# Kernel tuning notes

Hardware: AMD Instinct MI355X
Metric: run time of the kernel (lower is better)

The kernel has to match this reference:

```python
import jax, jax.numpy as jnp
import numpy as np

D_MODEL = 1024
N_EXPERTS = 8
TOP_K = 2
BOTTLENECK = 64
B, S = 2, 4096
ADAPTER_SCALE = 0.5


def setup_inputs() -> dict:
    key = jax.random.key(0)
    ks = jax.random.split(key, 8)
    sd = 0.02
    x = jax.random.normal(ks[0], (B, S, D_MODEL), dtype=jnp.float32)
    w_gate = jax.random.normal(ks[1], (D_MODEL, N_EXPERTS), dtype=jnp.float32) * sd
    w_noise = jax.random.normal(ks[2], (D_MODEL, N_EXPERTS), dtype=jnp.float32) * sd
    Wd = jax.random.normal(ks[3], (N_EXPERTS, D_MODEL, BOTTLENECK), dtype=jnp.float32) * sd
    bd = jnp.zeros((N_EXPERTS, BOTTLENECK), dtype=jnp.float32)
    Wu = jax.random.normal(ks[4], (N_EXPERTS, BOTTLENECK, D_MODEL), dtype=jnp.float32) * sd
    bu = jnp.zeros((N_EXPERTS, D_MODEL), dtype=jnp.float32)
    return {"x": x, "w_gate": w_gate, "w_noise": w_noise,
            "Wd": Wd, "bd": bd, "Wu": Wu, "bu": bu}


def _moe_forward(x, w_gate, w_noise, Wd, bd, Wu, bu):
    b, s, d = x.shape
    xf = x.reshape(-1, d)                      # [T, D] flattened tokens
    T = xf.shape[0]

    # --- noisy top-k gating (eval mode: no noise added, logits = clean) ---
    clean_logits = xf @ w_gate                 # [T, E]
    logits = clean_logits
    k1 = min(TOP_K + 1, N_EXPERTS)
    top_logits, top_idx = jax.lax.top_k(logits, k1)
    top_k_logits = top_logits[:, :TOP_K]       # [T, k]
    top_k_idx = top_idx[:, :TOP_K]             # [T, k]
    top_k_gates = jax.nn.softmax(top_k_logits, axis=-1)
    rows = jnp.arange(T)[:, None]
    gates = jnp.zeros((T, N_EXPERTS), dtype=top_k_gates.dtype)
    gates = gates.at[rows, top_k_idx].set(top_k_gates)  # sparse gate matrix [T, E]

    # --- experts (AdaptFormer adapters): dense compute, sparse combine ---
    # mathematically identical to SparseDispatcher dispatch/combine:
    # out[t] = sum_e gates[t,e] * expert_e(x[t])  (gates zero off top-k)
    h = jax.nn.relu(jnp.einsum('td,edb->teb', xf, Wd) + bd[None, :, :])  # [T,E,b]
    y = jnp.einsum('teb,ebd->ted', h, Wu) + bu[None, :, :]               # [T,E,D]
    y = ADAPTER_SCALE * y
    out = jnp.einsum('te,ted->td', gates, y)   # weighted combine (index_add equiv)
    return out.reshape(b, s, d)


def reference(x, w_gate, w_noise, Wd, bd, Wu, bu):
    return _moe_forward(x, w_gate, w_noise, Wd, bd, Wu, bu)
```

## Files before the change

kernel.cpp:

```cpp
#include <hip/hip_runtime.h>
#include <stdint.h>

#define T_TOK 8192
#define DM    1024
#define NE    8
#define BOT   64
#define HD    512
#define HD2   576
#define PW    8
#define NPREP (T_TOK / PW)

typedef __attribute__((ext_vector_type(8))) short bf16x8;
typedef __attribute__((ext_vector_type(4))) short bf16x4;
typedef __attribute__((ext_vector_type(4))) float f32x4;

__device__ __forceinline__ ushort f2bf(float f) {
  union { float f; uint32_t u; } v; v.f = f;
  uint32_t r = (v.u + 0x7fffu + ((v.u >> 16) & 1u)) >> 16;
  return (ushort)r;
}

__global__ __launch_bounds__(256, 2)
void prep_cvt_kernel(const float* __restrict__ x, const float* __restrict__ wg,
                     const float* __restrict__ Wd, const float* __restrict__ Wu,
                     const float* __restrict__ bu,
                     ushort* __restrict__ Xb, float* __restrict__ sg,
                     ushort* __restrict__ H2, ushort* __restrict__ WdT,
                     ushort* __restrict__ Wu2T) {
  __shared__ float part[4][PW][NE];
  __shared__ float sgl[PW][NE];
  __shared__ ushort tl[64][72];
  if (blockIdx.x < NPREP) {
    const int lane = threadIdx.x & 63;
    const int w    = threadIdx.x >> 6;
    const int t0   = blockIdx.x * PW;
    const int dd   = w * 256 + lane * 4;
    float4 wgr[4][2];
    #pragma unroll
    for (int j = 0; j < 4; ++j) {
      wgr[j][0] = *(const float4*)(wg + (size_t)(dd + j) * NE);
      wgr[j][1] = *(const float4*)(wg + (size_t)(dd + j) * NE + 4);
    }
    const int ebit = ((lane & 1) << 2) | (lane & 2) | ((lane >> 2) & 1);
    const float* xp = x + (size_t)t0 * DM + dd;
    float4 xv = *(const float4*)xp;
    #pragma unroll
    for (int tk = 0; tk < PW; ++tk) {
      float4 nxt = {};
      if (tk + 1 < PW) nxt = *(const float4*)(xp + (size_t)(tk + 1) * DM);
      bf16x4 xb;
      xb[0] = (short)f2bf(xv.x); xb[1] = (short)f2bf(xv.y);
      xb[2] = (short)f2bf(xv.z); xb[3] = (short)f2bf(xv.w);
      *(bf16x4*)(Xb + (size_t)(t0 + tk) * DM + dd) = xb;
      float a[NE] = {};
      const float* xs = (const float*)&xv;
      #pragma unroll
      for (int j = 0; j < 4; ++j) {
        const float xj = xs[j];
        const float* wr = (const float*)&wgr[j][0];
        #pragma unroll
        for (int e = 0; e < NE; ++e) a[e] += xj * wr[e];
      }
      float t0v[4];
      #pragma unroll
      for (int j = 0; j < 4; ++j) {
        float send = (lane & 1) ? a[j] : a[j + 4];
        float keep = (lane & 1) ? a[j + 4] : a[j];
        t0v[j] = keep + __shfl_xor(send, 1);
      }
      float t1v[2];
      #pragma unroll
      for (int j = 0; j < 2; ++j) {
        float send = (lane & 2) ? t0v[j] : t0v[j + 2];
        float keep = (lane & 2) ? t0v[j + 2] : t0v[j];
        t1v[j] = keep + __shfl_xor(send, 2);
      }
      {
        float send = (lane & 4) ? t1v[0] : t1v[1];
        float keep = (lane & 4) ? t1v[1] : t1v[0];
        float t2 = keep + __shfl_xor(send, 4);
        t2 += __shfl_xor(t2, 8);
        t2 += __shfl_xor(t2, 16);
        t2 += __shfl_xor(t2, 32);
        if (lane < NE) part[w][tk][ebit] = t2;
      }
      xv = nxt;
    }
    __syncthreads();
    const int tid = threadIdx.x;
    if (tid < PW) {
      float lg[NE];
      #pragma unroll
      for (int e = 0; e < NE; ++e)
        lg[e] = part[0][tid][e] + part[1][tid][e] + part[2][tid][e] + part[3][tid][e];
      int e0 = 0; float l0 = lg[0];
      #pragma unroll
      for (int e = 1; e < NE; ++e) if (lg[e] > l0) { l0 = lg[e]; e0 = e; }
      int e1 = -1; float l1 = -3.4e38f;
      #pragma unroll
      for (int e = 0; e < NE; ++e) if (e != e0 && lg[e] > l1) { l1 = lg[e]; e1 = e; }
      const float p1  = __expf(l1 - l0);
      const float inv = 1.f / (1.f + p1);
      const float g0 = 0.5f * inv, g1 = 0.5f * p1 * inv;
      float g[NE];
      #pragma unroll
      for (int e = 0; e < NE; ++e) g[e] = (e == e0) ? g0 : ((e == e1) ? g1 : 0.f);
      #pragma unroll
      for (int e = 0; e < NE; ++e) sgl[tid][e] = g[e];
      *(float4*)(sg + (size_t)(t0 + tid) * NE)     = *(float4*)&g[0];
      *(float4*)(sg + (size_t)(t0 + tid) * NE + 4) = *(float4*)&g[4];
    }
    __syncthreads();
    if (tid < PW * 8) {
      const int tk = tid >> 3, ch = tid & 7;
      bf16x8 v;
      #pragma unroll
      for (int k = 0; k < 8; ++k)
        v[k] = (ch == 0) ? (short)f2bf(sgl[tk][k]) : (short)0;
      *(bf16x8*)(H2 + (size_t)(t0 + tk) * HD2 + HD + ch * 8) = v;
    }
  } else {
    const int rr = threadIdx.x >> 2;
    const int cc = (threadIdx.x & 3) * 16;
    const int bx = blockIdx.x - NPREP;
    if (bx < 128) {
      const int e  = bx >> 4;
      const int d0 = (bx & 15) * 64;
      const float* src = Wd + ((size_t)e * DM + d0 + rr) * BOT + cc;
      #pragma unroll
      for (int i = 0; i < 4; ++i) {
        float4 v = *(const float4*)(src + i * 4);
        tl[rr][cc + i * 4 + 0] = f2bf(v.x);
        tl[rr][cc + i * 4 + 1] = f2bf(v.y);
        tl[rr][cc + i * 4 + 2] = f2bf(v.z);
        tl[rr][cc + i * 4 + 3] = f2bf(v.w);
      }
      __syncthreads();
      bf16x8 o0, o1;
      #pragma unroll
      for (int k = 0; k < 8; ++k) o0[k] = (short)tl[cc + k][rr];
      #pragma unroll
      for (int k = 0; k < 8; ++k) o1[k] = (short)tl[cc + 8 + k][rr];
      ushort* dst = WdT + ((size_t)e * BOT + rr) * DM + d0 + cc;
      *(bf16x8*)dst       = o0;
      *(bf16x8*)(dst + 8) = o1;
    } else {
      const int b2 = bx - 128;
      const int n0 = (b2 >> 4) * 64;
      const int d0 = (b2 & 15) * 64;
      const int n  = n0 + rr;
      #pragma unroll
      for (int i = 0; i < 4; ++i) {
        float4 v;
        if (n < HD)           v = *(const float4*)(Wu + (size_t)n * DM + d0 + cc + i * 4);
        else if (n < HD + NE) v = *(const float4*)(bu + (size_t)(n - HD) * DM + d0 + cc + i * 4);
        else { v.x = 0.f; v.y = 0.f; v.z = 0.f; v.w = 0.f; }
        tl[rr][cc + i * 4 + 0] = f2bf(v.x);
        tl[rr][cc + i * 4 + 1] = f2bf(v.y);
        tl[rr][cc + i * 4 + 2] = f2bf(v.z);
        tl[rr][cc + i * 4 + 3] = f2bf(v.w);
      }
      __syncthreads();
      bf16x8 o0, o1;
      #pragma unroll
      for (int k = 0; k < 8; ++k) o0[k] = (short)tl[cc + k][rr];
      #pragma unroll
      for (int k = 0; k < 8; ++k) o1[k] = (short)tl[cc + 8 + k][rr];
      ushort* dst = Wu2T + (size_t)(d0 + rr) * HD2 + n0 + cc;
      *(bf16x8*)dst       = o0;
      *(bf16x8*)(dst + 8) = o1;
    }
  }
}

template <int EPI, int NKT, int NBX>
__global__ __launch_bounds__(256)
void gemm_bt(const ushort* __restrict__ A, const ushort* __restrict__ B,
             const float* __restrict__ sg, const float* __restrict__ bd,
             ushort* __restrict__ Hout, float* __restrict__ Cout, int nwg) {
  constexpr int K = NKT * 64;
  __shared__ __attribute__((aligned(16))) ushort sA[3][128 * 64];
  __shared__ __attribute__((aligned(16))) ushort sB[3][64 * 64];
  const int lane = threadIdx.x & 63;
  const int w    = threadIdx.x >> 6;
  const int lb = (blockIdx.x % 8) * (nwg / 8) + blockIdx.x / 8;
  const int tile_m = (lb / NBX) * 128;
  const int tile_n = (lb % NBX) * 64;
  const int wm = (w >> 1) * 64;
  const int wn = (w & 1) * 32;
  const int sr = lane >> 3;
  const int sc = ((lane & 7) * 8) ^ (sr << 3);
  const int lr = lane & 15;
  const int kg = lane >> 4;
  const int swz = (lr & 7) << 3;
  f32x4 acc[4][2] = {};

#define STAGE(buf, kt) do {                                                       \
    const int k0_ = (kt) << 6;                                                    \
    _Pragma("unroll")                                                             \
    for (int c = 0; c < 4; ++c) {                                                 \
      const ushort* ga = A + (size_t)(tile_m + w * 32 + c * 8 + sr) * K + k0_ + sc; \
      __builtin_amdgcn_global_load_lds((const __attribute__((address_space(1))) void*)ga, \
          (__attribute__((address_space(3))) void*)&sA[buf][(w * 32 + c * 8) * 64], 16, 0, 0); \
    }                                                                             \
    _Pragma("unroll")                                                             \
    for (int c = 0; c < 2; ++c) {                                                 \
      const ushort* gb = B + (size_t)(tile_n + w * 16 + c * 8 + sr) * K + k0_ + sc; \
      __builtin_amdgcn_global_load_lds((const __attribute__((address_space(1))) void*)gb, \
          (__attribute__((address_space(3))) void*)&sB[buf][(w * 16 + c * 8) * 64], 16, 0, 0); \
    } } while (0)

  STAGE(0, 0);
  STAGE(1, 1);
  for (int kt = 0; kt < NKT; ++kt) {
    const int cur = kt % 3;
    if (kt + 2 < NKT) {
      STAGE((kt + 2) % 3, kt + 2);
      asm volatile("s_waitcnt vmcnt(12)" ::: "memory");
    } else if (kt + 1 < NKT) {
      asm volatile("s_waitcnt vmcnt(6)" ::: "memory");
    } else {
      asm volatile("s_waitcnt vmcnt(0)" ::: "memory");
    }
    __builtin_amdgcn_s_barrier();
    #pragma unroll
    for (int s = 0; s < 2; ++s) {
      bf16x8 af[4], bfr[2];
      #pragma unroll
      for (int i = 0; i < 4; ++i)
        af[i] = *(const bf16x8*)&sA[cur][(wm + i * 16 + lr) * 64 + ((s * 32 + kg * 8) ^ swz)];
      #pragma unroll
      for (int j = 0; j < 2; ++j)
        bfr[j] = *(const bf16x8*)&sB[cur][(wn + j * 16 + lr) * 64 + ((s * 32 + kg * 8) ^ swz)];
      #pragma unroll
      for (int i = 0; i < 4; ++i)
        #pragma unroll
        for (int j = 0; j < 2; ++j)
          acc[i][j] = __builtin_amdgcn_mfma_f32_16x16x32_bf16(af[i], bfr[j], acc[i][j], 0, 0, 0);
    }
    asm volatile("" ::: "memory");
    __builtin_amdgcn_s_barrier();
  }
#undef STAGE

  if (EPI == 0) {
    const int e = tile_n >> 6;
    float bdv[2];
    #pragma unroll
    for (int j = 0; j < 2; ++j) bdv[j] = bd[tile_n + wn + j * 16 + lr];
    #pragma unroll
    for (int i = 0; i < 4; ++i) {
      #pragma unroll
      for (int r = 0; r < 4; ++r) {
        const int t = tile_m + wm + i * 16 + kg * 4 + r;
        const float sglv = sg[(size_t)t * NE + e];
        #pragma unroll
        for (int j = 0; j < 2; ++j) {
          float v = fmaxf(acc[i][j][r] + bdv[j], 0.f) * sglv;
          Hout[(size_t)t * HD2 + tile_n + wn + j * 16 + lr] = f2bf(v);
        }
      }
    }
  } else {
    #pragma unroll
    for (int i = 0; i < 4; ++i) {
      #pragma unroll
      for (int r = 0; r < 4; ++r) {
        const int t = tile_m + wm + i * 16 + kg * 4 + r;
        #pragma unroll
        for (int j = 0; j < 2; ++j)
          Cout[(size_t)t * DM + tile_n + wn + j * 16 + lr] = acc[i][j][r];
      }
    }
  }
}

extern "C" void kernel_launch(void* const* d_in, const int* in_sizes, int n_in,
                              void* d_out, int out_size, void* d_ws, size_t ws_size,
                              hipStream_t stream) {
  const float* x  = (const float*)d_in[0];
  const float* wg = (const float*)d_in[1];
  const float* Wd = (const float*)d_in[3];
  const float* bd = (const float*)d_in[4];
  const float* Wu = (const float*)d_in[5];
  const float* bu = (const float*)d_in[6];
  float* out = (float*)d_out;

  char* ws = (char*)d_ws;
  ushort* Xb   = (ushort*)(ws);
  ushort* H2   = (ushort*)(ws + 16777216);
  ushort* WdT  = (ushort*)(ws + 26214400);
  ushort* Wu2T = (ushort*)(ws + 27262976);
  float*  sgw  = (float*) (ws + 28442624);

  prep_cvt_kernel<<<dim3(NPREP + 272), dim3(256), 0, stream>>>(
      x, wg, Wd, Wu, bu, Xb, sgw, H2, WdT, Wu2T);

  gemm_bt<0, 16, 8><<<dim3(512), dim3(256), 0, stream>>>(Xb, WdT, sgw, bd, H2, nullptr, 512);
  gemm_bt<1, 9, 16><<<dim3(1024), dim3(256), 0, stream>>>(H2, Wu2T, sgw, nullptr, nullptr, out, 1024);
}
```

Before: 50.38 us.

## Route tokens to top-2 experts and compute only selected adapter work

Replaces dense all-expert computation with sparse dispatch. A new routing kernel uses wave ballots and atomics to build per-expert token lists for the down-projection and per-expert-pair token lists for the up-projection. The down GEMM then runs only on routed tokens, and the up GEMM uses K=128 (two experts) instead of 576, with the gated bias applied in its epilogue. This removes roughly three quarters of the FLOPs, at the cost of an extra kernel launch, gathered (indirect) loads, atomics, and partially filled tiles. The GEMM loops also move the prefetch after compute, drop the trailing barrier, and add setprio around the MFMA instructions.

```diff
diff --git a/kernel.cpp b/kernel.cpp
--- a/kernel.cpp
+++ b/kernel.cpp
@@ -6,9 +6,19 @@
 #define NE    8
 #define BOT   64
 #define HD    512
-#define HD2   576
 #define PW    8
 #define NPREP (T_TOK / PW)
+
+#define XB_OFF   0u
+#define HC_OFF   16777216u
+#define WDT_OFF  18874368u
+#define WUT_OFF  19922944u
+#define SG_OFF   20971520u
+#define RT_OFF   21233664u
+#define IDX_OFF  21266432u
+#define SCL_OFF  21528576u
+#define PL_OFF   21790720u
+#define CNT_OFF  22708224u
 
 typedef __attribute__((ext_vector_type(8))) short bf16x8;
 typedef __attribute__((ext_vector_type(4))) short bf16x4;
@@ -23,14 +33,13 @@
 __global__ __launch_bounds__(256, 2)
 void prep_cvt_kernel(const float* __restrict__ x, const float* __restrict__ wg,
                      const float* __restrict__ Wd, const float* __restrict__ Wu,
-                     const float* __restrict__ bu,
                      ushort* __restrict__ Xb, float* __restrict__ sg,
-                     ushort* __restrict__ H2, ushort* __restrict__ WdT,
-                     ushort* __restrict__ Wu2T) {
+                     int* __restrict__ route, ushort* __restrict__ WdT,
+                     ushort* __restrict__ WuT, int* __restrict__ cntz) {
   __shared__ float part[4][PW][NE];
-  __shared__ float sgl[PW][NE];
   __shared__ ushort tl[64][72];
   if (blockIdx.x < NPREP) {
+    if (blockIdx.x == 0 && threadIdx.x < 36) cntz[threadIdx.x] = 0;
     const int lane = threadIdx.x & 63;
     const int w    = threadIdx.x >> 6;
     const int t0   = blockIdx.x * PW;
@@ -105,19 +114,10 @@
       float g[NE];
       #pragma unroll
       for (int e = 0; e < NE; ++e) g[e] = (e == e0) ? g0 : ((e == e1) ? g1 : 0.f);
-      #pragma unroll
-      for (int e = 0; e < NE; ++e) sgl[tid][e] = g[e];
       *(float4*)(sg + (size_t)(t0 + tid) * NE)     = *(float4*)&g[0];
       *(float4*)(sg + (size_t)(t0 + tid) * NE + 4) = *(float4*)&g[4];
-    }
-    __syncthreads();
-    if (tid < PW * 8) {
-      const int tk = tid >> 3, ch = tid & 7;
-      bf16x8 v;
-      #pragma unroll
-      for (int k = 0; k < 8; ++k)
-        v[k] = (ch == 0) ? (short)f2bf(sgl[tk][k]) : (short)0;
-      *(bf16x8*)(H2 + (size_t)(t0 + tk) * HD2 + HD + ch * 8) = v;
+      const int es0 = min(e0, e1), es1 = max(e0, e1);
+      route[t0 + tid] = es0 | (es1 << 4);
     }
   } else {
     const int rr = threadIdx.x >> 2;
@@ -148,13 +148,10 @@
       const int b2 = bx - 128;
       const int n0 = (b2 >> 4) * 64;
       const int d0 = (b2 & 15) * 64;
-      const int n  = n0 + rr;
+      const float* src = Wu + (size_t)(n0 + rr) * DM + d0 + cc;
       #pragma unroll
       for (int i = 0; i < 4; ++i) {
-        float4 v;
-        if (n < HD)           v = *(const float4*)(Wu + (size_t)n * DM + d0 + cc + i * 4);
-        else if (n < HD + NE) v = *(const float4*)(bu + (size_t)(n - HD) * DM + d0 + cc + i * 4);
-        else { v.x = 0.f; v.y = 0.f; v.z = 0.f; v.w = 0.f; }
+        float4 v = *(const float4*)(src + i * 4);
         tl[rr][cc + i * 4 + 0] = f2bf(v.x);
         tl[rr][cc + i * 4 + 1] = f2bf(v.y);
         tl[rr][cc + i * 4 + 2] = f2bf(v.z);
@@ -166,26 +163,86 @@
       for (int k = 0; k < 8; ++k) o0[k] = (short)tl[cc + k][rr];
       #pragma unroll
       for (int k = 0; k < 8; ++k) o1[k] = (short)tl[cc + 8 + k][rr];
-      ushort* dst = Wu2T + (size_t)(d0 + rr) * HD2 + n0 + cc;
+      ushort* dst = WuT + (size_t)(d0 + rr) * HD + n0 + cc;
       *(bf16x8*)dst       = o0;
       *(bf16x8*)(dst + 8) = o1;
     }
   }
 }
 
-template <int EPI, int NKT, int NBX>
 __global__ __launch_bounds__(256)
-void gemm_bt(const ushort* __restrict__ A, const ushort* __restrict__ B,
-             const float* __restrict__ sg, const float* __restrict__ bd,
-             ushort* __restrict__ Hout, float* __restrict__ Cout, int nwg) {
-  constexpr int K = NKT * 64;
+void route_kernel(const int* __restrict__ route, const float* __restrict__ sg,
+                  int* __restrict__ cnt, int* __restrict__ idx1,
+                  float* __restrict__ scl1, int* __restrict__ plist) {
+  int* pcnt = cnt + 8;
+  const int lane = threadIdx.x & 63;
+  const int w    = threadIdx.x >> 6;
+  const int t    = (blockIdx.x * 4 + w) * 64 + lane;
+  const int r    = route[t];
+  const int es0 = r & 15, es1 = (r >> 4) & 15;
+  const float g0 = sg[(size_t)t * NE + es0];
+  const float g1 = sg[(size_t)t * NE + es1];
+  const int p = es0 * 7 - ((es0 * (es0 - 1)) >> 1) + (es1 - es0 - 1);
+  const unsigned long long lower = (1ull << lane) - 1ull;
+  #pragma unroll
+  for (int e = 0; e < NE; ++e) {
+    unsigned long long m0 = __ballot(es0 == e);
+    unsigned long long m1 = __ballot(es1 == e);
+    unsigned long long mm = m0 | m1;
+    if (mm) {
+      const int c0 = __popcll(m0);
+      const int c  = c0 + __popcll(m1);
+      const int ldr = __ffsll((long long)mm) - 1;
+      int b = 0;
+      if (lane == ldr) b = atomicAdd(&cnt[e], c);
+      b = __shfl(b, ldr);
+      if (es0 == e) {
+        const int rk = __popcll(m0 & lower);
+        idx1[e * T_TOK + b + rk] = (t << 1);
+        scl1[e * T_TOK + b + rk] = g0;
+      }
+      if (es1 == e) {
+        const int rk = c0 + __popcll(m1 & lower);
+        idx1[e * T_TOK + b + rk] = (t << 1) | 1;
+        scl1[e * T_TOK + b + rk] = g1;
+      }
+    }
+  }
+  #pragma unroll
+  for (int pp = 0; pp < 28; ++pp) {
+    unsigned long long m = __ballot(p == pp);
+    if (m) {
+      const int c = __popcll(m);
+      const int ldr = __ffsll((long long)m) - 1;
+      int b = 0;
+      if (lane == ldr) b = atomicAdd(&pcnt[pp], c);
+      b = __shfl(b, ldr);
+      if (p == pp) plist[pp * T_TOK + b + __popcll(m & lower)] = t;
+    }
+  }
+}
+
+__global__ __launch_bounds__(256)
+void gemm1s(const ushort* __restrict__ Xb, const ushort* __restrict__ WdT,
+            const int* __restrict__ cnt, const int* __restrict__ idx1,
+            const float* __restrict__ scl1, const float* __restrict__ bd,
+            ushort* __restrict__ Hc) {
   __shared__ __attribute__((aligned(16))) ushort sA[3][128 * 64];
   __shared__ __attribute__((aligned(16))) ushort sB[3][64 * 64];
+  int e = -1, seg = 0, at = 0;
+  #pragma unroll
+  for (int ee = 0; ee < NE; ++ee) {
+    const int nt = (cnt[ee] + 127) >> 7;
+    if (e < 0 && (int)blockIdx.x < at + nt) { e = ee; seg = blockIdx.x - at; }
+    at += nt;
+  }
+  if (e < 0) return;
+  const int ne    = cnt[e];
+  const int rbase = seg * 128;
+  const int lbase = e * T_TOK + rbase;
+  const int nval  = min(128, ne - rbase);
   const int lane = threadIdx.x & 63;
   const int w    = threadIdx.x >> 6;
-  const int lb = (blockIdx.x % 8) * (nwg / 8) + blockIdx.x / 8;
-  const int tile_m = (lb / NBX) * 128;
-  const int tile_n = (lb % NBX) * 64;
   const int wm = (w >> 1) * 64;
   const int wn = (w & 1) * 32;
   const int sr = lane >> 3;
@@ -193,36 +250,37 @@
   const int lr = lane & 15;
   const int kg = lane >> 4;
   const int swz = (lr & 7) << 3;
+  int atok[4];
+  #pragma unroll
+  for (int c = 0; c < 4; ++c) {
+    const int rr = w * 32 + c * 8 + sr;
+    atok[c] = idx1[lbase + (rr < nval ? rr : 0)] >> 1;
+  }
   f32x4 acc[4][2] = {};
 
-#define STAGE(buf, kt) do {                                                       \
+#define STAGE1(buf, kt) do {                                                      \
     const int k0_ = (kt) << 6;                                                    \
     _Pragma("unroll")                                                             \
     for (int c = 0; c < 4; ++c) {                                                 \
-      const ushort* ga = A + (size_t)(tile_m + w * 32 + c * 8 + sr) * K + k0_ + sc; \
+      const ushort* ga = Xb + (size_t)atok[c] * DM + k0_ + sc;                    \
       __builtin_amdgcn_global_load_lds((const __attribute__((address_space(1))) void*)ga, \
           (__attribute__((address_space(3))) void*)&sA[buf][(w * 32 + c * 8) * 64], 16, 0, 0); \
     }                                                                             \
     _Pragma("unroll")                                                             \
     for (int c = 0; c < 2; ++c) {                                                 \
-      const ushort* gb = B + (size_t)(tile_n + w * 16 + c * 8 + sr) * K + k0_ + sc; \
+      const ushort* gb = WdT + (size_t)(e * 64 + w * 16 + c * 8 + sr) * DM + k0_ + sc; \
       __builtin_amdgcn_global_load_lds((const __attribute__((address_space(1))) void*)gb, \
           (__attribute__((address_space(3))) void*)&sB[buf][(w * 16 + c * 8) * 64], 16, 0, 0); \
     } } while (0)
 
-  STAGE(0, 0);
-  STAGE(1, 1);
-  for (int kt = 0; kt < NKT; ++kt) {
+  STAGE1(0, 0);
+  STAGE1(1, 1);
+  for (int kt = 0; kt < 16; ++kt) {
     const int cur = kt % 3;
-    if (kt + 2 < NKT) {
-      STAGE((kt + 2) % 3, kt + 2);
-      asm volatile("s_waitcnt vmcnt(12)" ::: "memory");
-    } else if (kt + 1 < NKT) {
-      asm volatile("s_waitcnt vmcnt(6)" ::: "memory");
-    } else {
-      asm volatile("s_waitcnt vmcnt(0)" ::: "memory");
-    }
+    if (kt + 1 < 16) asm volatile("s_waitcnt vmcnt(6)" ::: "memory");
+    else             asm volatile("s_waitcnt vmcnt(0)" ::: "memory");
     __builtin_amdgcn_s_barrier();
+    asm volatile("" ::: "memory");
     #pragma unroll
     for (int s = 0; s < 2; ++s) {
       bf16x8 af[4], bfr[2];
@@ -232,44 +290,156 @@
       #pragma unroll
       for (int j = 0; j < 2; ++j)
         bfr[j] = *(const bf16x8*)&sB[cur][(wn + j * 16 + lr) * 64 + ((s * 32 + kg * 8) ^ swz)];
+      __builtin_amdgcn_s_setprio(1);
       #pragma unroll
       for (int i = 0; i < 4; ++i)
         #pragma unroll
         for (int j = 0; j < 2; ++j)
           acc[i][j] = __builtin_amdgcn_mfma_f32_16x16x32_bf16(af[i], bfr[j], acc[i][j], 0, 0, 0);
+      __builtin_amdgcn_s_setprio(0);
     }
     asm volatile("" ::: "memory");
-    __builtin_amdgcn_s_barrier();
-  }
-#undef STAGE
-
-  if (EPI == 0) {
-    const int e = tile_n >> 6;
-    float bdv[2];
+    if (kt + 2 < 16) STAGE1((kt + 2) % 3, kt + 2);
+  }
+#undef STAGE1
+
+  float bdv[2];
+  #pragma unroll
+  for (int j = 0; j < 2; ++j) bdv[j] = bd[e * BOT + wn + j * 16 + lr];
+  #pragma unroll
+  for (int i = 0; i < 4; ++i) {
     #pragma unroll
-    for (int j = 0; j < 2; ++j) bdv[j] = bd[tile_n + wn + j * 16 + lr];
-    #pragma unroll
-    for (int i = 0; i < 4; ++i) {
-      #pragma unroll
-      for (int r = 0; r < 4; ++r) {
-        const int t = tile_m + wm + i * 16 + kg * 4 + r;
-        const float sglv = sg[(size_t)t * NE + e];
+    for (int r = 0; r < 4; ++r) {
+      const int rl = wm + i * 16 + kg * 4 + r;
+      if (rl < nval) {
+        const int en  = idx1[lbase + rl];
+        const float s = scl1[lbase + rl];
+        ushort* hp = Hc + (size_t)(en >> 1) * 128 + (en & 1) * 64;
         #pragma unroll
         for (int j = 0; j < 2; ++j) {
-          float v = fmaxf(acc[i][j][r] + bdv[j], 0.f) * sglv;
-          Hout[(size_t)t * HD2 + tile_n + wn + j * 16 + lr] = f2bf(v);
+          const float v = fmaxf(acc[i][j][r] + bdv[j], 0.f) * s;
+          hp[wn + j * 16 + lr] = f2bf(v);
         }
       }
     }
-  } else {
+  }
+}
+
+__global__ __launch_bounds__(256)
+void gemm2s(const ushort* __restrict__ Hc, const ushort* __restrict__ WuT,
+            const int* __restrict__ cnt, const int* __restrict__ plist,
+            const float* __restrict__ sg, const float* __restrict__ bu,
+            float* __restrict__ out, int nwg) {
+  __shared__ __attribute__((aligned(16))) ushort sA[2][128 * 64];
+  __shared__ __attribute__((aligned(16))) ushort sB[2][64 * 64];
+  const int* pcnt = cnt + 8;
+  const int lb = (blockIdx.x % 8) * (nwg / 8) + blockIdx.x / 8;
+  const int mt = lb >> 4;
+  const int tile_n = (lb & 15) * 64;
+  int p = -1, seg = 0, at = 0;
+  #pragma unroll
+  for (int pp = 0; pp < 28; ++pp) {
+    const int nt = (pcnt[pp] + 127) >> 7;
+    if (p < 0 && mt < at + nt) { p = pp; seg = mt - at; }
+    at += nt;
+  }
+  if (p < 0) return;
+  int es0 = 0, es1 = 1, a2 = 0;
+  #pragma unroll
+  for (int a = 0; a < NE; ++a) {
+    const int ca = 7 - a;
+    if (p >= a2 && p < a2 + ca) { es0 = a; es1 = a + 1 + (p - a2); }
+    a2 += ca;
+  }
+  const int np    = pcnt[p];
+  const int rbase = seg * 128;
+  const int lbase = p * T_TOK + rbase;
+  const int nval  = min(128, np - rbase);
+  const int lane = threadIdx.x & 63;
+  const int w    = threadIdx.x >> 6;
+  const int wm = (w >> 1) * 64;
+  const int wn = (w & 1) * 32;
+  const int sr = lane >> 3;
+  const int sc = ((lane & 7) * 8) ^ (sr << 3);
+  const int lr = lane & 15;
+  const int kg = lane >> 4;
+  const int swz = (lr & 7) << 3;
+  int atok[4];
+  #pragma unroll
+  for (int c = 0; c < 4; ++c) {
+    const int rr = w * 32 + c * 8 + sr;
+    atok[c] = plist[lbase + (rr < nval ? rr : 0)];
+  }
+  const int bc0 = es0 * 64, bc1 = es1 * 64;
+  f32x4 acc[4][2] = {};
+
+#define STAGE2(buf, kt, bc) do {                                                  \
+    _Pragma("unroll")                                                             \
+    for (int c = 0; c < 4; ++c) {                                                 \
+      const ushort* ga = Hc + (size_t)atok[c] * 128 + (kt) * 64 + sc;             \
+      __builtin_amdgcn_global_load_lds((const __attribute__((address_space(1))) void*)ga, \
+          (__attribute__((address_space(3))) void*)&sA[buf][(w * 32 + c * 8) * 64], 16, 0, 0); \
+    }                                                                             \
+    _Pragma("unroll")                                                             \
+    for (int c = 0; c < 2; ++c) {                                                 \
+      const ushort* gb = WuT + (size_t)(tile_n + w * 16 + c * 8 + sr) * HD + (bc) + sc; \
+      __builtin_amdgcn_global_load_lds((const __attribute__((address_space(1))) void*)gb, \
+          (__attribute__((address_space(3))) void*)&sB[buf][(w * 16 + c * 8) * 64], 16, 0, 0); \
+    } } while (0)
+
+#define COMPUTE2(cur) do {                                                        \
+    _Pragma("unroll")                                                             \
+    for (int s = 0; s < 2; ++s) {                                                 \
+      bf16x8 af[4], bfr[2];                                                       \
+      _Pragma("unroll")                                                           \
+      for (int i = 0; i < 4; ++i)                                                 \
+        af[i] = *(const bf16x8*)&sA[cur][(wm + i * 16 + lr) * 64 + ((s * 32 + kg * 8) ^ swz)]; \
+      _Pragma("unroll")                                                           \
+      for (int j = 0; j < 2; ++j)                                                 \
+        bfr[j] = *(const bf16x8*)&sB[cur][(wn + j * 16 + lr) * 64 + ((s * 32 + kg * 8) ^ swz)]; \
+      __builtin_amdgcn_s_setprio(1);                                              \
+      _Pragma("unroll")                                                           \
+      for (int i = 0; i < 4; ++i)                                                 \
+        _Pragma("unroll")                                                         \
+        for (int j = 0; j < 2; ++j)                                               \
+          acc[i][j] = __builtin_amdgcn_mfma_f32_16x16x32_bf16(af[i], bfr[j], acc[i][j], 0, 0, 0); \
+      __builtin_amdgcn_s_setprio(0);                                              \
+    } } while (0)
+
+  STAGE2(0, 0, bc0);
+  STAGE2(1, 1, bc1);
+  asm volatile("s_waitcnt vmcnt(6)" ::: "memory");
+  __builtin_amdgcn_s_barrier();
+  asm volatile("" ::: "memory");
+  COMPUTE2(0);
+  asm volatile("s_waitcnt vmcnt(0)" ::: "memory");
+  __builtin_amdgcn_s_barrier();
+  asm volatile("" ::: "memory");
+  COMPUTE2(1);
+#undef STAGE2
+#undef COMPUTE2
+
+  float bu0[2], bu1[2];
+  #pragma unroll
+  for (int j = 0; j < 2; ++j) {
+    const int col = tile_n + wn + j * 16 + lr;
+    bu0[j] = bu[(size_t)es0 * DM + col];
+    bu1[j] = bu[(size_t)es1 * DM + col];
+  }
+  #pragma unroll
+  for (int i = 0; i < 4; ++i) {
     #pragma unroll
-    for (int i = 0; i < 4; ++i) {
-      #pragma unroll
-      for (int r = 0; r < 4; ++r) {
-        const int t = tile_m + wm + i * 16 + kg * 4 + r;
+    for (int r = 0; r < 4; ++r) {
+      const int rl = wm + i * 16 + kg * 4 + r;
+      if (rl < nval) {
+        const int tok = plist[lbase + rl];
+        const float g0 = sg[(size_t)tok * NE + es0];
+        const float g1 = sg[(size_t)tok * NE + es1];
         #pragma unroll
-        for (int j = 0; j < 2; ++j)
-          Cout[(size_t)t * DM + tile_n + wn + j * 16 + lr] = acc[i][j][r];
+        for (int j = 0; j < 2; ++j) {
+          const int col = tile_n + wn + j * 16 + lr;
+          out[(size_t)tok * DM + col] = acc[i][j][r] + g0 * bu0[j] + g1 * bu1[j];
+        }
       }
     }
   }
@@ -287,15 +457,23 @@
   float* out = (float*)d_out;
 
   char* ws = (char*)d_ws;
-  ushort* Xb   = (ushort*)(ws);
-  ushort* H2   = (ushort*)(ws + 16777216);
-  ushort* WdT  = (ushort*)(ws + 26214400);
-  ushort* Wu2T = (ushort*)(ws + 27262976);
-  float*  sgw  = (float*) (ws + 28442624);
-
-  prep_cvt_kernel<<<dim3(NPREP + 272), dim3(256), 0, stream>>>(
-      x, wg, Wd, Wu, bu, Xb, sgw, H2, WdT, Wu2T);
-
-  gemm_bt<0, 16, 8><<<dim3(512), dim3(256), 0, stream>>>(Xb, WdT, sgw, bd, H2, nullptr, 512);
-  gemm_bt<1, 9, 16><<<dim3(1024), dim3(256), 0, stream>>>(H2, Wu2T, sgw, nullptr, nullptr, out, 1024);
-}
+  ushort* Xb    = (ushort*)(ws + XB_OFF);
+  ushort* Hc    = (ushort*)(ws + HC_OFF);
+  ushort* WdT   = (ushort*)(ws + WDT_OFF);
+  ushort* WuT   = (ushort*)(ws + WUT_OFF);
+  float*  sgw   = (float*) (ws + SG_OFF);
+  int*    route = (int*)   (ws + RT_OFF);
+  int*    idx1  = (int*)   (ws + IDX_OFF);
+  float*  scl1  = (float*) (ws + SCL_OFF);
+  int*    plist = (int*)   (ws + PL_OFF);
+  int*    cnt   = (int*)   (ws + CNT_OFF);
+
+  prep_cvt_kernel<<<dim3(NPREP + 256), dim3(256), 0, stream>>>(
+      x, wg, Wd, Wu, Xb, sgw, route, WdT, WuT, cnt);
+  route_kernel<<<dim3(32), dim3(256), 0, stream>>>(
+      route, sgw, cnt, idx1, scl1, plist);
+  gemm1s<<<dim3(136), dim3(256), 0, stream>>>(
+      Xb, WdT, cnt, idx1, scl1, bd, Hc);
+  gemm2s<<<dim3(1472), dim3(256), 0, stream>>>(
+      Hc, WuT, cnt, plist, sgw, bu, out, 1472);
+}
```

New measurement: 104.6 us. 108% more time.
